# Optimization experiments

Hardware: AMD Instinct MI355X
Metric: run time of the kernel (lower is better)

## Reference

```python
import jax, jax.numpy as jnp
import numpy as np

INPUT_SIZE = 128   # kernel is always launched with self.input_size -> only first 128 cols of x/w_ih used
HIDDEN = 256
NUM_LAYERS = 6
SEQ_LEN = 512
BATCH = 10


def _gru_scan(gates_x, w_hh, h0):
    """gates_x: (S, B, 3H) precomputed input contribution; w_hh: (3H, H)."""
    H = h0.shape[-1]

    def step(h, gx):
        gh = h @ w_hh.T                      # (B, 3H)
        rx, zx, nx = gx[..., :H], gx[..., H:2 * H], gx[..., 2 * H:]
        rh, zh, nh = gh[..., :H], gh[..., H:2 * H], gh[..., 2 * H:]
        r = jax.nn.sigmoid(rx + rh)
        z = jax.nn.sigmoid(zx + zh)
        n = jnp.tanh(nx + r * nh)
        h_new = (1.0 - z) * n + z * h
        return h_new, h_new

    _, out = jax.lax.scan(step, h0, gates_x)
    return out                                # (S, B, H)


def _forward(x, w_ih_l0, w_ih_rest, w_hh):
    S, B, _ = x.shape
    h0 = jnp.zeros((B, HIDDEN), dtype=x.dtype)
    layer_input = x
    for layer in range(NUM_LAYERS):
        # Faithful to the Triton launch: only the first INPUT_SIZE features are consumed.
        xs = layer_input[..., :INPUT_SIZE]                     # (S, B, 128)
        if layer == 0:
            wf = w_ih_l0[0][:, :INPUT_SIZE]
            wb = w_ih_l0[1][:, :INPUT_SIZE]
        else:
            wf = w_ih_rest[layer - 1, 0][:, :INPUT_SIZE]
            wb = w_ih_rest[layer - 1, 1][:, :INPUT_SIZE]
        gates_f = jnp.einsum('sbi,gi->sbg', xs, wf)            # (S, B, 3H)
        gates_b = jnp.einsum('sbi,gi->sbg', xs[::-1], wb)      # reversed time order
        fwd_out = _gru_scan(gates_f, w_hh[layer, 0], h0)       # (S, B, H)
        # torch code stores backward states time-aligned then flips; scan over
        # reversed input without re-flipping reproduces that flipped output.
        bwd_out = _gru_scan(gates_b, w_hh[layer, 1], h0)       # (S, B, H)
        layer_input = jnp.concatenate([fwd_out, bwd_out], axis=-1)  # (S, B, 2H)
    return layer_input                                          # last layer only


def setup_inputs() -> dict:
    key = jax.random.key(0)
    k1, k2, k3, k4 = jax.random.split(key, 4)
    x = jax.random.normal(k1, (SEQ_LEN, BATCH, INPUT_SIZE), dtype=jnp.float32)
    w_ih_l0 = jax.random.normal(k2, (2, 3 * HIDDEN, INPUT_SIZE), dtype=jnp.float32) * 0.05
    w_ih_rest = jax.random.normal(k3, (NUM_LAYERS - 1, 2, 3 * HIDDEN, 2 * HIDDEN), dtype=jnp.float32) * 0.05
    w_hh = jax.random.normal(k4, (NUM_LAYERS, 2, 3 * HIDDEN, HIDDEN), dtype=jnp.float32) * 0.05
    return {"x": x, "w_ih_l0": w_ih_l0, "w_ih_rest": w_ih_rest, "w_hh": w_hh}


def reference(x, w_ih_l0, w_ih_rest, w_hh):
    return _forward(x, w_ih_l0, w_ih_rest, w_hh)
```

## Files before the change

kernel.cpp:

```cpp
#include <hip/hip_runtime.h>
#include <stdint.h>


typedef short short8 __attribute__((ext_vector_type(8)));
typedef float floatx4 __attribute__((ext_vector_type(4)));
typedef unsigned long long u64;
typedef unsigned int u32;
typedef unsigned short u16;

#define SEQ 512

#define GSLOT_U64 4096
#define GRING_U64 (7 * 32 * GSLOT_U64)
#define HH_U16 (5 * 512 * 2048)
#define TAGS_OFF_B ((size_t)GRING_U64 * 8 + (size_t)HH_U16 * 2)

#define RZ_OFF(col, quad)  (((col)*32 + (quad)*8) ^ ((((col)>>2)&3)<<3))
#define NX_OFF(j, quad)    (16384 + (((j)*64 + (quad)*16) ^ ((((j)>>1)&3)<<4)))

__device__ __forceinline__ u16 f2bf(float f){ union{float f;u32 i;}v; v.f=f; u32 u=v.i; u += 0x7fffu + ((u>>16)&1u); return (u16)(u>>16); }
__device__ __forceinline__ float bf2f(u16 h){ union{u32 i;float f;}v; v.i=((u32)h)<<16; return v.f; }
__device__ __forceinline__ short8 ld8f(const float* p){
    float4 a=*(const float4*)p, b=*(const float4*)(p+4);
    short8 r; r[0]=(short)f2bf(a.x); r[1]=(short)f2bf(a.y); r[2]=(short)f2bf(a.z); r[3]=(short)f2bf(a.w);
    r[4]=(short)f2bf(b.x); r[5]=(short)f2bf(b.y); r[6]=(short)f2bf(b.z); r[7]=(short)f2bf(b.w); return r;
}
__device__ __forceinline__ short8 pk2(u64 a, u64 b){ union{u64 q[2]; short8 s;}v; v.q[0]=a; v.q[1]=b; return v.s; }
__device__ __forceinline__ u64 pack4bf(floatx4 a){
    return (u64)f2bf(a[0]) | ((u64)f2bf(a[1])<<16) | ((u64)f2bf(a[2])<<32) | ((u64)f2bf(a[3])<<48);
}
__device__ __forceinline__ float rcp_(float x){ float r; asm("v_rcp_f32 %0, %1" : "=v"(r) : "v"(x)); return r; }
__device__ __forceinline__ float sigmoidf_(float x){ return rcp_(1.0f + __expf(-x)); }
__device__ __forceinline__ float tanhf_(float x){ return 1.0f - 2.0f*rcp_(__expf(2.0f*x) + 1.0f); }

#define ALD(p)    __hip_atomic_load((p), __ATOMIC_RELAXED, __HIP_MEMORY_SCOPE_AGENT)
#define AST(p,v)  __hip_atomic_store((p),(v),__ATOMIC_RELAXED,__HIP_MEMORY_SCOPE_AGENT)
__device__ __forceinline__ void wait_vm0(){ asm volatile("s_waitcnt vmcnt(0)" ::: "memory"); }
#define WVC(n) asm volatile("s_waitcnt vmcnt(" #n ")" ::: "memory")
__device__ __forceinline__ void lgkm_barrier(){ asm volatile("s_waitcnt lgkmcnt(0)\n\ts_barrier" ::: "memory"); }

__device__ __forceinline__ void st16_sc1(void* p, floatx4 v){
    asm volatile("global_store_dwordx4 %0, %1, off sc1" :: "v"(p), "v"(v) : "memory");
}
__device__ __forceinline__ void dma16(const void* g, void* l) {
    __builtin_amdgcn_global_load_lds(
        reinterpret_cast<const __attribute__((address_space(1))) unsigned int*>(
            (uintptr_t)g),
        reinterpret_cast<__attribute__((address_space(3))) unsigned int*>(
            (uintptr_t)l), 16, 0, 16);
}
__device__ __forceinline__ void dma4(const void* g, void* l) {
    __builtin_amdgcn_global_load_lds(
        reinterpret_cast<const __attribute__((address_space(1))) unsigned int*>(
            (uintptr_t)g),
        reinterpret_cast<__attribute__((address_space(3))) unsigned int*>(
            (uintptr_t)l), 4, 0, 16);
}

__global__ __launch_bounds__(512, 2)
void gru_pipeline(const float* __restrict__ x,
                  const float* __restrict__ wihl0,
                  const float* __restrict__ wihrest,
                  const float* __restrict__ whh,
                  float* __restrict__ out,
                  u64* __restrict__ gring,
                  u16* __restrict__ hhb,
                  u32* __restrict__ tags)
{
    __shared__ u64 smem_[14404];
    const int blk  = blockIdx.x;
    const int tid  = threadIdx.x;
    const int w    = tid >> 6;
    const int lane = tid & 63;
    const int n16  = lane & 15;
    const int quad = lane >> 4;
    u32* cparr = tags + 2816;

    if (blk < 7) {
        const int s = blk;
        const int wu = __builtin_amdgcn_readfirstlane(tid) >> 6;
        const int layer = (s==6)?5:s, dir=(s==6)?1:0;
        const float* whhp = whh + ((size_t)(layer*2+dir))*768*256;

        short8 bh[6][8];
#pragma unroll
        for (int g=0; g<3; ++g)
#pragma unroll
        for (int u=0; u<2; ++u) {
            const int row = g*256 + 32*w + 16*u + n16;
#pragma unroll
            for (int q=0; q<8; ++q)
                bh[g*2+u][q] = ld8f(whhp + (size_t)row*256 + q*32 + quad*8);
        }

        char* gb   = (char*)smem_;
        u16*  hbuf = (u16*)(gb + 98304);
        u32*  tagmir = (u32*)((char*)smem_ + 115200);
        for (int i=tid; i<8448; i+=512) hbuf[i] = 0;

        u32* gtp = tags + s*32;
        u32* htp = tags + 256 + s*512;

        {
            int gd=0;
            while (ALD(gtp + 0) != 1u){ if(++gd>3000000) break; __builtin_amdgcn_s_sleep(2); }
            const char* sg = (const char*)(gring + (size_t)(s*32)*GSLOT_U64);
#pragma unroll
            for (int r=0; r<4; ++r) dma16(sg + (r*512+tid)*16, gb + (r*512+tid)*16);
            gd=0;
            while (ALD(gtp + 1) != 2u){ if(++gd>3000000) break; __builtin_amdgcn_s_sleep(2); }
            sg = (const char*)(gring + (size_t)(s*32 + 1)*GSLOT_U64);
#pragma unroll
            for (int r=0; r<4; ++r) dma16(sg + (r*512+tid)*16, gb + 32768 + (r*512+tid)*16);
            if (tid==0) { dma4(gtp + 2, tagmir + 2); dma4(gtp + 3, tagmir + 3); }
            wait_vm0(); lgkm_barrier();
        }

        for (int t=0; t<SEQ; ++t) {
            const u16* hbP = hbuf + (t&1)*4224;
            if (wu == 0) {
                if ((t&3)==0) AST(cparr + s, (u32)(t+1));
                if (s<=4 && t>=4) AST(htp + (t-4), (u32)(t-3));
            }
            if (t+2 < SEQ) {
                if (tagmir[(t+2)&3] != (u32)(t+3)) {
                    int gd=0;
                    while (ALD(gtp + ((t+2)&31)) != (u32)(t+3)){ if(++gd>3000000) break; __builtin_amdgcn_s_sleep(1); }
                }
                if (wu==0 && lane==0 && t+4 < SEQ)
                    dma4(gtp + ((t+4)&31), tagmir + ((t+4)&3));
                const char* sg = (const char*)(gring + (size_t)(s*32 + ((t+2)&31))*GSLOT_U64);
                char* dg = gb + ((t+2)%3)*32768;
#pragma unroll
                for (int r=0; r<4; ++r) dma16(sg + (r*512+tid)*16, dg + (r*512+tid)*16);
            }

            if (t >= 1) {
                if (s<=4) {
                    if (wu < 4) {
                        const int b = tid & 15, k = (tid >> 4) & 15;
                        char* hq = (char*)(hhb + (size_t)s*1048576 + (size_t)(t-1)*2048);
                        st16_sc1(hq + b*256 + k*16, *(const floatx4*)(hbP + b*264 + 8*k));
                    }
                } else {
                    const int off = (s==6)?256:0;
                    {
                        const int b = tid >> 6, jg = (tid & 63)*4;
                        union { u64 q; u16 h[4]; } v; v.q = *(const u64*)(hbP + b*264 + jg);
                        float4 o; o.x=bf2f(v.h[0]); o.y=bf2f(v.h[1]); o.z=bf2f(v.h[2]); o.w=bf2f(v.h[3]);
                        *(float4*)(out + (size_t)(t-1)*5120 + (size_t)b*512 + off + jg) = o;
                    }
                    if (wu < 2) {
                        const int idx = tid + 512;
                        const int b = idx >> 6, jg = (idx & 63)*4;
                        union { u64 q; u16 h[4]; } v; v.q = *(const u64*)(hbP + b*264 + jg);
                        float4 o; o.x=bf2f(v.h[0]); o.y=bf2f(v.h[1]); o.z=bf2f(v.h[2]); o.w=bf2f(v.h[3]);
                        *(float4*)(out + (size_t)(t-1)*5120 + (size_t)b*512 + off + jg) = o;
                    }
                }
            }
            const char* g0 = gb + (t%3)*32768;
            floatx4 acc[6];
#pragma unroll
            for (int g=0; g<2; ++g)
#pragma unroll
            for (int u=0; u<2; ++u) {
                const int col = g*256 + 32*w + 16*u + n16;
                const u64 gw = *(const u64*)(g0 + RZ_OFF(col, quad));
#pragma unroll
                for (int r=0; r<4; ++r) acc[g*2+u][r] = bf2f((u16)(gw >> (16*r)));
            }
            acc[4] = (floatx4){0.f,0.f,0.f,0.f};
            acc[5] = (floatx4){0.f,0.f,0.f,0.f};
#pragma unroll
            for (int q=0; q<8; ++q) {
                short8 ah = *(const short8*)(hbP + n16*264 + q*32 + quad*8);
#pragma unroll
                for (int m=0; m<6; ++m)
                    acc[m] = __builtin_amdgcn_mfma_f32_16x16x32_bf16(ah, bh[m][q], acc[m], 0,0,0);
            }
            u16* hbN = hbuf + ((t+1)&1)*4224;
#pragma unroll
            for (int u=0; u<2; ++u) {
                const int j = 32*w + 16*u + n16;
                const floatx4 nx4 = *(const floatx4*)(g0 + NX_OFF(j, quad));
#pragma unroll
                for (int r=0; r<4; ++r) {
                    const int b = quad*4 + r;
                    float rr = sigmoidf_(acc[u][r]);
                    float zz = sigmoidf_(acc[2+u][r]);
                    float nn = tanhf_(nx4[r] + rr*acc[4+u][r]);
                    float hp = bf2f(hbP[b*264 + j]);
                    float hn = nn + zz*(hp - nn);
                    hbN[b*264 + j] = f2bf(hn);
                }
            }
            if (t < 4 || t >= SEQ-5) {
                wait_vm0();
            } else if (s <= 4) {
                if (wu == 0)      { WVC(8); }
                else if (wu < 4)  { WVC(6); }
                else              { WVC(4); }
            } else {
                if (wu == 0)      { WVC(9); }
                else if (wu == 1) { WVC(8); }
                else              { WVC(6); }
            }
            lgkm_barrier();
        }
        const u16* hbL = hbuf;
        if (s<=4) {
            if (wu < 4) {
                const int b = tid & 15, k = (tid >> 4) & 15;
                char* hq = (char*)(hhb + (size_t)s*1048576 + (size_t)(SEQ-1)*2048);
                st16_sc1(hq + b*256 + k*16, *(const floatx4*)(hbL + b*264 + 8*k));
            }
        } else {
            const int off = (s==6)?256:0;
            {
                const int b = tid >> 6, jg = (tid & 63)*4;
                union { u64 q; u16 h[4]; } v; v.q = *(const u64*)(hbL + b*264 + jg);
                float4 o; o.x=bf2f(v.h[0]); o.y=bf2f(v.h[1]); o.z=bf2f(v.h[2]); o.w=bf2f(v.h[3]);
                *(float4*)(out + (size_t)(SEQ-1)*5120 + (size_t)b*512 + off + jg) = o;
            }
            if (wu < 2) {
                const int idx = tid + 512;
                const int b = idx >> 6, jg = (idx & 63)*4;
                union { u64 q; u16 h[4]; } v; v.q = *(const u64*)(hbL + b*264 + jg);
                float4 o; o.x=bf2f(v.h[0]); o.y=bf2f(v.h[1]); o.z=bf2f(v.h[2]); o.w=bf2f(v.h[3]);
                *(float4*)(out + (size_t)(SEQ-1)*5120 + (size_t)b*512 + off + jg) = o;
            }
        }
        wait_vm0(); lgkm_barrier();
        if (tid==0 && s<=4) {
            AST(htp + 508, 509u); AST(htp + 509, 510u);
            AST(htp + 510, 511u); AST(htp + 511, 512u);
        }
        return;
    }

    int sh, t0;
    if (blk < 10)      { sh = 0;               t0 = blk - 7;      }
    else if (blk < 25) { sh = 1 + (blk-10)/3;  t0 = (blk-10)%3;   }
    else               { sh = 6;               t0 = blk - 25;     }

    const int layer = (sh==6)?5:sh, dir=(sh==6)?1:0;
    const float* wihp; int stride;
    if (layer==0){ wihp = wihl0 + (size_t)dir*768*128; stride=128; }
    else         { wihp = wihrest + ((size_t)((layer-1)*2+dir))*768*512; stride=512; }

    short8 bxf[6][4];
#pragma unroll
    for (int i=0; i<6; ++i) {
        const int col = (w*6+i)*16 + n16;
#pragma unroll
        for (int q=0; q<4; ++q)
            bxf[i][q] = ld8f(wihp + (size_t)col*stride + q*32 + quad*8);
    }
    char* tb = (char*)smem_;
    const int bmA = (n16>9)?9:n16;
    const int lsrc = (sh==6)? 4 : (sh-1);
    u32* gtp_sh = tags + sh*32;

    int tprev = -1;
    for (int t = t0; t < SEQ; t += 3) {
        if (t >= 32) {
            int gd=0;
            while ((int)ALD(cparr + sh) < t-24){ if(++gd>1000000) break; __builtin_amdgcn_s_sleep(8); }
        }
        if (tprev >= 0) {
            wait_vm0();
            __syncthreads();
            if (tid==0) AST(gtp_sh + (tprev&31), (u32)(tprev+1));
        }
        short8 ax[4];
        if (sh == 0) {
            const float* xr = x + (size_t)t*1280 + (size_t)bmA*128;
#pragma unroll
            for (int q=0; q<4; ++q) ax[q] = ld8f(xr + q*32 + quad*8);
        } else {
            const int srct = (sh==6)? (SEQ-1-t) : t;
            int gd=0;
            while (ALD(tags + 256 + lsrc*512 + srct) != (u32)(srct+1)){ if(++gd>3000000) break; __builtin_amdgcn_s_sleep(4); }
            const u64* hq = (const u64*)(hhb + (size_t)lsrc*1048576 + (size_t)srct*2048);
#pragma unroll
            for (int q=0; q<4; ++q) {
                u64 a = ALD(hq + n16*32 + q*8 + quad*2);
                u64 b = ALD(hq + n16*32 + q*8 + quad*2 + 1);
                ax[q] = pk2(a, b);
            }
        }
        floatx4 acc[6];
#pragma unroll
        for (int i=0; i<6; ++i) acc[i] = (floatx4){0.f,0.f,0.f,0.f};
#pragma unroll
        for (int q=0; q<4; ++q)
#pragma unroll
            for (int i=0; i<6; ++i)
                acc[i] = __builtin_amdgcn_mfma_f32_16x16x32_bf16(ax[q], bxf[i][q], acc[i], 0,0,0);

#pragma unroll
        for (int i=0; i<6; ++i) {
            const int col = (w*6+i)*16 + n16;
            if (col < 512) *(u64*)(tb + RZ_OFF(col, quad)) = pack4bf(acc[i]);
            else           *(floatx4*)(tb + NX_OFF(col-512, quad)) = acc[i];
        }
        __syncthreads();
        char* gq = (char*)(gring + (size_t)(sh*32 + (t&31))*GSLOT_U64);
#pragma unroll
        for (int k=0;k<4;++k)
            st16_sc1(gq + tid*64 + k*16, *(const floatx4*)((const char*)tb + tid*64 + k*16));
        tprev = t;
    }
    wait_vm0(); __syncthreads();
    if (tid==0 && tprev>=0) AST(gtp_sh + (tprev&31), (u32)(tprev+1));
}

extern "C" void kernel_launch(void* const* d_in, const int* in_sizes, int n_in,
                              void* d_out, int out_size, void* d_ws, size_t ws_size,
                              hipStream_t stream) {
    (void)in_sizes; (void)n_in; (void)out_size; (void)ws_size;
    const float* x       = (const float*)d_in[0];
    const float* wihl0   = (const float*)d_in[1];
    const float* wihrest = (const float*)d_in[2];
    const float* whh     = (const float*)d_in[3];
    float* out = (float*)d_out;
    u64* gring = (u64*)d_ws;
    u16* hhb   = (u16*)((char*)d_ws + (size_t)GRING_U64*8);
    u32* tags  = (u32*)((char*)d_ws + TAGS_OFF_B);

    gru_pipeline<<<dim3(28), dim3(512), 0, stream>>>(x, wihl0, wihrest, whh, out,
                                                     gring, hhb, tags);
}
```

Baseline: 3.301 ms.

## Split recurrent block waves into gate-prefetch and h-store/flag-publish groups

Warp-specializes the recurrent scan block: waves 0-3 do all gate-ring prefetch DMAs (8 chunks per thread instead of 4), and waves 4-7 do the hidden-state stores to global or the output and publish the progress tags. The per-wave vmcnt waits are simplified, so each group waits only on its own outstanding memory operations. The goal is to take memory traffic and flag publishing off the critical path of the compute waves. The tradeoff is an uneven memory load per wave, and the tag publish now waits on vmcnt in the store waves, which changes the ordering between producer and consumer.

After: 3.039 ms. 1.09x faster.

```diff
diff --git a/kernel.cpp b/kernel.cpp
--- a/kernel.cpp
+++ b/kernel.cpp
@@ -104,25 +104,25 @@
         {
             int gd=0;
             while (ALD(gtp + 0) != 1u){ if(++gd>3000000) break; __builtin_amdgcn_s_sleep(2); }
-            const char* sg = (const char*)(gring + (size_t)(s*32)*GSLOT_U64);
-#pragma unroll
-            for (int r=0; r<4; ++r) dma16(sg + (r*512+tid)*16, gb + (r*512+tid)*16);
+            if (tid < 256) {
+                const char* sg = (const char*)(gring + (size_t)(s*32)*GSLOT_U64);
+#pragma unroll
+                for (int r=0; r<8; ++r) dma16(sg + (r*256+tid)*16, gb + (r*256+tid)*16);
+            }
             gd=0;
             while (ALD(gtp + 1) != 2u){ if(++gd>3000000) break; __builtin_amdgcn_s_sleep(2); }
-            sg = (const char*)(gring + (size_t)(s*32 + 1)*GSLOT_U64);
-#pragma unroll
-            for (int r=0; r<4; ++r) dma16(sg + (r*512+tid)*16, gb + 32768 + (r*512+tid)*16);
+            if (tid < 256) {
+                const char* sg = (const char*)(gring + (size_t)(s*32 + 1)*GSLOT_U64);
+#pragma unroll
+                for (int r=0; r<8; ++r) dma16(sg + (r*256+tid)*16, gb + 32768 + (r*256+tid)*16);
+            }
             if (tid==0) { dma4(gtp + 2, tagmir + 2); dma4(gtp + 3, tagmir + 3); }
             wait_vm0(); lgkm_barrier();
         }
 
         for (int t=0; t<SEQ; ++t) {
             const u16* hbP = hbuf + (t&1)*4224;
-            if (wu == 0) {
-                if ((t&3)==0) AST(cparr + s, (u32)(t+1));
-                if (s<=4 && t>=4) AST(htp + (t-4), (u32)(t-3));
-            }
-            if (t+2 < SEQ) {
+            if (t+2 < SEQ && wu < 4) {
                 if (tagmir[(t+2)&3] != (u32)(t+3)) {
                     int gd=0;
                     while (ALD(gtp + ((t+2)&31)) != (u32)(t+3)){ if(++gd>3000000) break; __builtin_amdgcn_s_sleep(1); }
@@ -132,30 +132,30 @@
                 const char* sg = (const char*)(gring + (size_t)(s*32 + ((t+2)&31))*GSLOT_U64);
                 char* dg = gb + ((t+2)%3)*32768;
 #pragma unroll
-                for (int r=0; r<4; ++r) dma16(sg + (r*512+tid)*16, dg + (r*512+tid)*16);
-            }
-
-            if (t >= 1) {
+                for (int r=0; r<8; ++r) dma16(sg + (r*256+tid)*16, dg + (r*256+tid)*16);
+            }
+            if (wu == 4) {
+                if (s<=4 && t>=4) { WVC(4); AST(htp + (t-4), (u32)(t-3)); }
+                if ((t&3)==0) AST(cparr + s, (u32)(t+1));
+            }
+
+            if (t >= 1 && wu >= 4) {
                 if (s<=4) {
-                    if (wu < 4) {
-                        const int b = tid & 15, k = (tid >> 4) & 15;
-                        char* hq = (char*)(hhb + (size_t)s*1048576 + (size_t)(t-1)*2048);
-                        st16_sc1(hq + b*256 + k*16, *(const floatx4*)(hbP + b*264 + 8*k));
-                    }
+                    const int idx = tid - 256;
+                    const int b = idx & 15, k = (idx >> 4) & 15;
+                    char* hq = (char*)(hhb + (size_t)s*1048576 + (size_t)(t-1)*2048);
+                    st16_sc1(hq + b*256 + k*16, *(const floatx4*)(hbP + b*264 + 8*k));
                 } else {
                     const int off = (s==6)?256:0;
-                    {
-                        const int b = tid >> 6, jg = (tid & 63)*4;
-                        union { u64 q; u16 h[4]; } v; v.q = *(const u64*)(hbP + b*264 + jg);
-                        float4 o; o.x=bf2f(v.h[0]); o.y=bf2f(v.h[1]); o.z=bf2f(v.h[2]); o.w=bf2f(v.h[3]);
-                        *(float4*)(out + (size_t)(t-1)*5120 + (size_t)b*512 + off + jg) = o;
-                    }
-                    if (wu < 2) {
-                        const int idx = tid + 512;
-                        const int b = idx >> 6, jg = (idx & 63)*4;
-                        union { u64 q; u16 h[4]; } v; v.q = *(const u64*)(hbP + b*264 + jg);
-                        float4 o; o.x=bf2f(v.h[0]); o.y=bf2f(v.h[1]); o.z=bf2f(v.h[2]); o.w=bf2f(v.h[3]);
-                        *(float4*)(out + (size_t)(t-1)*5120 + (size_t)b*512 + off + jg) = o;
+#pragma unroll
+                    for (int k=0;k<3;++k) {
+                        const int idx = (tid-256) + 256*k;
+                        if (idx < 640) {
+                            const int b = idx >> 6, jg = (idx & 63)*4;
+                            union { u64 q; u16 h[4]; } v; v.q = *(const u64*)(hbP + b*264 + jg);
+                            float4 o; o.x=bf2f(v.h[0]); o.y=bf2f(v.h[1]); o.z=bf2f(v.h[2]); o.w=bf2f(v.h[3]);
+                            *(float4*)(out + (size_t)(t-1)*5120 + (size_t)b*512 + off + jg) = o;
+                        }
                     }
                 }
             }
@@ -197,38 +197,32 @@
             }
             if (t < 4 || t >= SEQ-5) {
                 wait_vm0();
-            } else if (s <= 4) {
-                if (wu == 0)      { WVC(8); }
-                else if (wu < 4)  { WVC(6); }
-                else              { WVC(4); }
-            } else {
-                if (wu == 0)      { WVC(9); }
-                else if (wu == 1) { WVC(8); }
-                else              { WVC(6); }
+            } else if (wu == 0) {
+                WVC(9);
+            } else if (wu < 4) {
+                WVC(8);
             }
             lgkm_barrier();
         }
         const u16* hbL = hbuf;
-        if (s<=4) {
-            if (wu < 4) {
-                const int b = tid & 15, k = (tid >> 4) & 15;
+        if (wu >= 4) {
+            if (s<=4) {
+                const int idx = tid - 256;
+                const int b = idx & 15, k = (idx >> 4) & 15;
                 char* hq = (char*)(hhb + (size_t)s*1048576 + (size_t)(SEQ-1)*2048);
                 st16_sc1(hq + b*256 + k*16, *(const floatx4*)(hbL + b*264 + 8*k));
-            }
-        } else {
-            const int off = (s==6)?256:0;
-            {
-                const int b = tid >> 6, jg = (tid & 63)*4;
-                union { u64 q; u16 h[4]; } v; v.q = *(const u64*)(hbL + b*264 + jg);
-                float4 o; o.x=bf2f(v.h[0]); o.y=bf2f(v.h[1]); o.z=bf2f(v.h[2]); o.w=bf2f(v.h[3]);
-                *(float4*)(out + (size_t)(SEQ-1)*5120 + (size_t)b*512 + off + jg) = o;
-            }
-            if (wu < 2) {
-                const int idx = tid + 512;
-                const int b = idx >> 6, jg = (idx & 63)*4;
-                union { u64 q; u16 h[4]; } v; v.q = *(const u64*)(hbL + b*264 + jg);
-                float4 o; o.x=bf2f(v.h[0]); o.y=bf2f(v.h[1]); o.z=bf2f(v.h[2]); o.w=bf2f(v.h[3]);
-                *(float4*)(out + (size_t)(SEQ-1)*5120 + (size_t)b*512 + off + jg) = o;
+            } else {
+                const int off = (s==6)?256:0;
+#pragma unroll
+                for (int k=0;k<3;++k) {
+                    const int idx = (tid-256) + 256*k;
+                    if (idx < 640) {
+                        const int b = idx >> 6, jg = (idx & 63)*4;
+                        union { u64 q; u16 h[4]; } v; v.q = *(const u64*)(hbL + b*264 + jg);
+                        float4 o; o.x=bf2f(v.h[0]); o.y=bf2f(v.h[1]); o.z=bf2f(v.h[2]); o.w=bf2f(v.h[3]);
+                        *(float4*)(out + (size_t)(SEQ-1)*5120 + (size_t)b*512 + off + jg) = o;
+                    }
+                }
             }
         }
         wait_vm0(); lgkm_barrier();
```
